# Kernel tuning notes

Measured on AMD Instinct MI355X. Metric: run time of the kernel, lower is better.

Reference implementation:

```python
import jax, jax.numpy as jnp
import numpy as np

T = 2048           # tokens (single prefill sequence)
HIDDEN = 2048
H = 16             # num heads
D_NOPE = 128
D_ROPE = 64
D_V = 128
KV_LORA = 512
EPS = 1e-6
ROPE_THETA = 10000.0


def setup_inputs() -> dict:
    key = jax.random.key(0)
    ks = jax.random.split(key, 7)
    s = 0.02
    return {
        "positions": jnp.arange(T, dtype=jnp.int64) if jax.config.jax_enable_x64 else jnp.arange(T, dtype=jnp.int32),
        "hidden_states": jax.random.normal(ks[0], (T, HIDDEN), dtype=jnp.float32),
        "w_q": jax.random.normal(ks[1], (HIDDEN, H * (D_NOPE + D_ROPE)), dtype=jnp.float32) * s,
        "w_kv_a": jax.random.normal(ks[2], (HIDDEN, KV_LORA + D_ROPE), dtype=jnp.float32) * s,
        "kv_a_ln_w": jax.random.uniform(ks[3], (KV_LORA,), dtype=jnp.float32, minval=0.5, maxval=1.5),
        "w_kv_b": jax.random.normal(ks[4], (KV_LORA, H * (D_NOPE + D_V)), dtype=jnp.float32) * s,
        "w_o": jax.random.normal(ks[5], (H * D_V, HIDDEN), dtype=jnp.float32) * s,
    }


def _rms_norm(x, w):
    var = jnp.mean(jnp.square(x), axis=-1, keepdims=True)
    return x * jax.lax.rsqrt(var + EPS) * w


def _rope_nonneox(x, positions):
    # x: [..., D_ROPE], GPT-J (interleaved) style rotation
    inv_freq = 1.0 / (ROPE_THETA ** (jnp.arange(0, D_ROPE, 2, dtype=jnp.float32) / D_ROPE))
    freqs = positions.astype(jnp.float32)[:, None] * inv_freq  # [T, D_ROPE//2]
    cos, sin = jnp.cos(freqs), jnp.sin(freqs)
    # broadcast over head dim if present
    while cos.ndim < x.ndim:
        cos, sin = cos[:, None], sin[:, None]
    x1, x2 = x[..., 0::2], x[..., 1::2]
    o1 = x1 * cos - x2 * sin
    o2 = x2 * cos + x1 * sin
    return jnp.stack([o1, o2], axis=-1).reshape(x.shape)


def reference(positions, hidden_states, w_q, w_kv_a, kv_a_ln_w, w_kv_b, w_o):
    scaling = (D_NOPE + D_ROPE) ** -0.5
    # q projection (q_lora_rank is None branch)
    q = (hidden_states @ w_q).reshape(T, H, D_NOPE + D_ROPE)
    q_nope, q_pe = q[..., :D_NOPE], q[..., D_NOPE:]
    # compressed KV latent
    latent = hidden_states @ w_kv_a                 # [T, KV_LORA + D_ROPE]
    kv_a = _rms_norm(latent[:, :KV_LORA], kv_a_ln_w)
    k_pe = latent[:, KV_LORA:]                      # [T, D_ROPE], shared across heads
    # decompress to per-head k_nope and v (kv_b_proj)
    kv = (kv_a @ w_kv_b).reshape(T, H, D_NOPE + D_V)
    k_nope, v = kv[..., :D_NOPE], kv[..., D_NOPE:]
    # non-neox RoPE
    q_pe = _rope_nonneox(q_pe, positions)
    k_pe = _rope_nonneox(k_pe, positions)           # [T, D_ROPE]
    # concat rope parts (k_pe broadcast over heads)
    q_full = jnp.concatenate([q_nope, q_pe], axis=-1)                         # [T,H,192]
    k_full = jnp.concatenate([k_nope, jnp.broadcast_to(k_pe[:, None, :], (T, H, D_ROPE))], axis=-1)
    # causal MHA
    scores = jnp.einsum("qhd,khd->hqk", q_full, k_full) * scaling
    causal = positions[:, None] >= positions[None, :]
    scores = jnp.where(causal[None], scores, -jnp.inf)
    attn = jax.nn.softmax(scores, axis=-1)
    out = jnp.einsum("hqk,khd->qhd", attn, v).reshape(T, H * D_V)
    return out @ w_o
```

## Files before the change

kernel.cpp:

```cpp
#include <hip/hip_runtime.h>
#include <hip/hip_bf16.h>
#include <stdint.h>

#define T_SEQ   2048
#define NHEAD   16
#define NPAD1   3712

typedef short bf16x8  __attribute__((ext_vector_type(8)));
typedef float f32x4   __attribute__((ext_vector_type(4)));
typedef float f32x16  __attribute__((ext_vector_type(16)));

__device__ __forceinline__ unsigned short f2bf(float f) {
  union { float f; uint32_t u; } v; v.f = f;
  uint32_t u = v.u;
  uint32_t r = u + 0x7FFF + ((u >> 16) & 1);
  return (unsigned short)(r >> 16);
}

__device__ __forceinline__ void async16(const void* g, void* l) {
  __builtin_amdgcn_global_load_lds(
      (const __attribute__((address_space(1))) void*)g,
      (__attribute__((address_space(3))) void*)l, 16, 0, 0);
}

__device__ __forceinline__ void tr32(const float* __restrict__ in,
    unsigned short* __restrict__ out, int R, int C, int bx, int by,
    float (*tile)[33], int tid) {
  int r0 = bx * 32, c0 = by * 32;
  int tx = tid & 31, ty = tid >> 5;
  for (int i = 0; i < 4; i++)
    tile[ty + i * 8][tx] = in[(size_t)(r0 + ty + i * 8) * C + c0 + tx];
  __syncthreads();
  for (int i = 0; i < 4; i++) {
    int c = ty + i * 8;
    out[(size_t)(c0 + c) * R + r0 + tx] = f2bf(tile[tx][c]);
  }
}

__global__ __launch_bounds__(256) void prep_kernel(
    const float* __restrict__ hs, const float* __restrict__ w_q,
    const float* __restrict__ w_kv_a, const float* __restrict__ w_kv_b,
    const float* __restrict__ w_o, const int* __restrict__ positions,
    unsigned short* __restrict__ hs_bf, unsigned short* __restrict__ wcat_t,
    unsigned short* __restrict__ wkvb_t, unsigned short* __restrict__ wo_t,
    float* __restrict__ rope_tab) {
  __shared__ float tile[32][33];
  int bid = blockIdx.x, tid = threadIdx.x;
  if (bid < 4096) {
    int i = (bid * 256 + tid) * 4;
    float4 v = *(const float4*)(hs + i);
    ushort4 o; o.x = f2bf(v.x); o.y = f2bf(v.y); o.z = f2bf(v.z); o.w = f2bf(v.w);
    *(ushort4*)(hs_bf + i) = o;
  } else if (bid < 4096 + 6144) {
    int l = bid - 4096;
    tr32(w_q, wcat_t, 2048, 3072, l & 63, l >> 6, tile, tid);
  } else if (bid < 4096 + 6144 + 1152) {
    int l = bid - (4096 + 6144);
    tr32(w_kv_a, wcat_t + (size_t)3072 * 2048, 2048, 576, l & 63, l >> 6, tile, tid);
  } else if (bid < 4096 + 6144 + 1152 + 2048) {
    int l = bid - (4096 + 6144 + 1152);
    tr32(w_kv_b, wkvb_t, 512, 4096, l & 15, l >> 4, tile, tid);
  } else if (bid < 4096 + 6144 + 1152 + 2048 + 4096) {
    int l = bid - (4096 + 6144 + 1152 + 2048);
    tr32(w_o, wo_t, 2048, 2048, l & 63, l >> 6, tile, tid);
  } else if (bid < 17600) {
    int l = bid - (4096 + 6144 + 1152 + 2048 + 4096);
    uint4 z = (uint4){0, 0, 0, 0};
    *(uint4*)(wcat_t + (size_t)3648 * 2048 + (size_t)(l * 256 + tid) * 8) = z;
  } else {
    int l = bid - 17600;
    int t = l * 8 + (tid >> 5), p = tid & 31;
    float pos = (float)positions[t];
    float inv_freq = powf(10000.f, -(float)(2 * p) / 64.f);
    float c, s; sincosf(pos * inv_freq, &s, &c);
    rope_tab[(size_t)t * 64 + 2 * p]     = c;
    rope_tab[(size_t)t * 64 + 2 * p + 1] = s;
  }
}

template<int TM, int EPI>
__global__ __launch_bounds__(256) void gemm_bt_kernel(
    const unsigned short* __restrict__ A, const unsigned short* __restrict__ B,
    void* __restrict__ Cv, int M, int N, int K,
    unsigned short* __restrict__ q_full, const float* __restrict__ rope_tab) {
  constexpr int MT = TM / 32;
  __shared__ __align__(16) unsigned short Asm[2][TM * 32];
  __shared__ __align__(16) unsigned short Bsm[2][128 * 32];
  int tid = threadIdx.x, wid = tid >> 6, lane = tid & 63;
  int lrow = lane & 15, lquad = lane >> 4;
  int m0 = blockIdx.x * TM, n0 = blockIdx.y * 128;
  int wm = (wid & 1) * (TM / 2), wn = (wid >> 1) * 64;

  int row_s = tid >> 2, cc_s = tid & 3;
  const unsigned short* Ag0 = A + (size_t)(m0 + row_s) * K + cc_s * 8;
  const unsigned short* Ag1 = A + (size_t)(m0 + row_s + 64) * K + cc_s * 8;
  const unsigned short* Bg0 = B + (size_t)(n0 + row_s) * K + cc_s * 8;
  const unsigned short* Bg1 = B + (size_t)(n0 + row_s + 64) * K + cc_s * 8;

  f32x4 acc[MT][4];
  #pragma unroll
  for (int i = 0; i < MT; i++)
    #pragma unroll
    for (int j = 0; j < 4; j++) acc[i][j] = (f32x4){0.f,0.f,0.f,0.f};

  async16(Ag0, &Asm[0][tid * 8]);
  if (TM == 128) async16(Ag1, &Asm[0][2048 + tid * 8]);
  async16(Bg0, &Bsm[0][tid * 8]);
  async16(Bg1, &Bsm[0][2048 + tid * 8]);

  int cur = 0;
  for (int k0 = 0; k0 < K; k0 += 32) {
    __syncthreads();
    if (k0 + 32 < K) {
      int nxt = cur ^ 1, kk = k0 + 32;
      async16(Ag0 + kk, &Asm[nxt][tid * 8]);
      if (TM == 128) async16(Ag1 + kk, &Asm[nxt][2048 + tid * 8]);
      async16(Bg0 + kk, &Bsm[nxt][tid * 8]);
      async16(Bg1 + kk, &Bsm[nxt][2048 + tid * 8]);
    }
    const unsigned short* As = Asm[cur];
    const unsigned short* Bs = Bsm[cur];
    bf16x8 af[MT], bfr[4];
    #pragma unroll
    for (int mt = 0; mt < MT; mt++)
      af[mt] = *(const bf16x8*)(As + (wm + mt * 16 + lrow) * 32 + lquad * 8);
    #pragma unroll
    for (int nt = 0; nt < 4; nt++)
      bfr[nt] = *(const bf16x8*)(Bs + (wn + nt * 16 + lrow) * 32 + lquad * 8);
    #pragma unroll
    for (int mt = 0; mt < MT; mt++)
      #pragma unroll
      for (int nt = 0; nt < 4; nt++)
        acc[mt][nt] = __builtin_amdgcn_mfma_f32_16x16x32_bf16(af[mt], bfr[nt], acc[mt][nt], 0, 0, 0);
    cur ^= 1;
  }

  if constexpr (EPI == 2) {
    const float scaling = 0.07216878364870323f;
    float* qlat = (float*)Cv;
    #pragma unroll
    for (int nt = 0; nt < 4; nt++) {
      int colb = n0 + wn + nt * 16;
      if (colb >= 3072) {
        int col = colb - 3072 + lrow;
        #pragma unroll
        for (int mt = 0; mt < MT; mt++) {
          int row = m0 + wm + mt * 16 + lquad * 4;
          #pragma unroll
          for (int r = 0; r < 4; r++)
            qlat[(size_t)(row + r) * 640 + col] = acc[mt][nt][r];
        }
      } else {
        int h = colb / 192;
        int hm = colb - h * 192;
        unsigned short* qh = q_full + (size_t)h * T_SEQ * 192;
        if (hm < 128) {
          #pragma unroll
          for (int mt = 0; mt < MT; mt++) {
            int row = m0 + wm + mt * 16 + lquad * 4;
            #pragma unroll
            for (int r = 0; r < 4; r++)
              qh[(size_t)(row + r) * 192 + hm + lrow] = f2bf(acc[mt][nt][r] * scaling);
          }
        } else {
          int p2 = (hm - 128 + lrow) & ~1;
          int odd = lrow & 1;
          #pragma unroll
          for (int mt = 0; mt < MT; mt++) {
            int row = m0 + wm + mt * 16 + lquad * 4;
            #pragma unroll
            for (int r = 0; r < 4; r++) {
              int rg = row + r;
              float c = rope_tab[(size_t)rg * 64 + p2];
              float s = rope_tab[(size_t)rg * 64 + p2 + 1];
              float own = acc[mt][nt][r];
              float oth = __shfl_xor(own, 1, 64);
              float o = odd ? (own * c + oth * s)
                            : (own * c - oth * s);
              qh[(size_t)rg * 192 + hm + lrow] = f2bf(o * scaling);
            }
          }
        }
      }
    }
  } else {
    #pragma unroll
    for (int mt = 0; mt < MT; mt++)
      #pragma unroll
      for (int nt = 0; nt < 4; nt++) {
        int row = m0 + wm + mt * 16 + lquad * 4;
        int col = n0 + wn + nt * 16 + lrow;
        #pragma unroll
        for (int r = 0; r < 4; r++) {
          if (EPI == 1)
            ((unsigned short*)Cv)[(size_t)(row + r) * N + col] = f2bf(acc[mt][nt][r]);
          else
            ((float*)Cv)[(size_t)(row + r) * N + col] = acc[mt][nt][r];
        }
      }
  }
}

__global__ __launch_bounds__(256) void postproc1_kernel(
    const float* __restrict__ q_lat,
    const float* __restrict__ ln_w,
    const float* __restrict__ rope_tab,
    unsigned short* __restrict__ kv_a,
    unsigned short* __restrict__ k_pe)
{
  int t = blockIdx.x, tid = threadIdx.x;
  const float* row = q_lat + (size_t)t * 640;

  float v0 = row[tid], v1 = row[256 + tid];
  float ss = v0 * v0 + v1 * v1;
  for (int m = 1; m < 64; m <<= 1) ss += __shfl_xor(ss, m, 64);
  __shared__ float red[4];
  if ((tid & 63) == 0) red[tid >> 6] = ss;
  __shared__ float kro[64];
  if (tid < 32) {
    float c = rope_tab[(size_t)t * 64 + 2 * tid];
    float s = rope_tab[(size_t)t * 64 + 2 * tid + 1];
    float x1 = row[512 + 2 * tid], x2 = row[512 + 2 * tid + 1];
    kro[2 * tid]     = x1 * c - x2 * s;
    kro[2 * tid + 1] = x2 * c + x1 * s;
  }
  __syncthreads();
  float rstd = rsqrtf((red[0] + red[1] + red[2] + red[3]) * (1.f / 512.f) + 1e-6f);
  kv_a[(size_t)t * 512 + tid]       = f2bf(v0 * rstd * ln_w[tid]);
  kv_a[(size_t)t * 512 + 256 + tid] = f2bf(v1 * rstd * ln_w[256 + tid]);
  if (tid < 64) k_pe[(size_t)t * 64 + tid] = f2bf(kro[tid]);
}

__global__ __launch_bounds__(256) void kvpost_kernel(
    const unsigned short* __restrict__ kv_b,
    unsigned short* __restrict__ v_t) {
  __shared__ unsigned short tile[32][41];
  int l = blockIdx.x, tid = threadIdx.x;
  int h = l >> 8, t0 = (l & 63) * 32, d0 = ((l >> 6) & 3) * 32;
  int tx = tid & 31, ty = tid >> 5;
  for (int i = 0; i < 4; i++)
    tile[ty + i * 8][tx] = kv_b[(size_t)(t0 + ty + i * 8) * 4096 + h * 256 + 128 + d0 + tx];
  __syncthreads();
  for (int i = 0; i < 4; i++)
    v_t[((size_t)h * 128 + d0 + ty + i * 8) * T_SEQ + t0 + tx] = tile[tx][ty + i * 8];
}

#define PP 76
__global__ __launch_bounds__(256, 2) void flash_kernel(
    const unsigned short* __restrict__ q_full,
    const unsigned short* __restrict__ kv_b,
    const unsigned short* __restrict__ k_pe,
    const unsigned short* __restrict__ v_t,
    unsigned short* __restrict__ attn_out)
{
  __shared__ __align__(16) unsigned short Ksm[2][1536 * 8];
  __shared__ __align__(16) unsigned short Vsm[1024 * 8];
  __shared__ __align__(16) unsigned short Psm[64 * PP];
  __shared__ float Lred[2][64];
  int h = blockIdx.x;
  int y = blockIdx.y;
  int qb = (y < 16) ? (31 - y) : (y - 16);
  int tid = threadIdx.x, wid = tid >> 6, lane = tid & 63;
  int l31 = lane & 31, l5 = lane >> 5, x7 = l31 & 7;
  int rq = wid & 1, kq = wid >> 1;

  const unsigned short* vh = v_t + (size_t)h * 128 * T_SEQ;

  const unsigned short* pK[6]; int sK[6];
  #pragma unroll
  for (int j = 0; j < 6; j++) {
    int s = tid + j * 256, row = s / 24, cm = s - row * 24;
    int c = cm ^ (row & 7);
    if (c < 16) { pK[j] = kv_b + (size_t)row * 4096 + h * 256 + c * 8; sK[j] = 64 * 4096; }
    else        { pK[j] = k_pe + (size_t)row * 64 + (c - 16) * 8;      sK[j] = 64 * 64; }
  }
  int gV[4];
  #pragma unroll
  for (int j = 0; j < 4; j++) {
    int s = tid + j * 256, d = s >> 3;
    gV[j] = d * T_SEQ + ((s & 7) ^ (d & 7)) * 8;
  }
  int kxo[12];
  #pragma unroll
  for (int kc = 0; kc < 12; kc++)
    kxo[kc] = (kq * 32 + l31) * 192 + ((kc * 2 + l5) ^ x7) * 8;
  int vxb[2];
  #pragma unroll
  for (int ntv = 0; ntv < 2; ntv++) vxb[ntv] = (kq * 64 + ntv * 32 + l31) * 64;

  bf16x8 qf[12];
  {
    const unsigned short* qrow =
        q_full + ((size_t)h * T_SEQ + qb * 64 + rq * 32 + l31) * 192 + l5 * 8;
    #pragma unroll
    for (int kc = 0; kc < 12; kc++) qf[kc] = *(const bf16x8*)(qrow + kc * 16);
  }
  f32x16 oacc[2];
  for (int i = 0; i < 2; i++) oacc[i] = (f32x16)(0.f);
  float lsum[16];
  #pragma unroll
  for (int r = 0; r < 16; r++) lsum[r] = 0.f;
  int rl[16];
  #pragma unroll
  for (int r = 0; r < 16; r++) rl[r] = (r & 3) + 8 * (r >> 2) + 4 * l5;

  #pragma unroll
  for (int j = 0; j < 6; j++) async16(pK[j], &Ksm[0][(tid + j * 256) * 8]);

  int cur = 0;
  for (int kb = 0; kb <= qb; kb++) {
    __syncthreads();
    {
      const unsigned short* vb = vh + kb * 64;
      #pragma unroll
      for (int j = 0; j < 4; j++) async16(vb + gV[j], &Vsm[(tid + j * 256) * 8]);
    }
    const unsigned short* Ks = Ksm[cur];
    f32x16 sacc = (f32x16)(0.f);
    #pragma unroll
    for (int kc = 0; kc < 12; kc++) {
      bf16x8 kf = *(const bf16x8*)(Ks + kxo[kc]);
      sacc = __builtin_amdgcn_mfma_f32_32x32x16_bf16(qf[kc], kf, sacc, 0, 0, 0);
    }
    if (kb == qb) {
      int col_g = kb * 64 + kq * 32 + l31;
      int row_b = qb * 64 + rq * 32;
      #pragma unroll
      for (int r = 0; r < 16; r++)
        if (col_g > row_b + rl[r]) sacc[r] = -1e30f;
    }
    #pragma unroll
    for (int r = 0; r < 16; r++) {
      float p = __expf(sacc[r]);
      sacc[r] = p;
      lsum[r] += p;
    }
    #pragma unroll
    for (int r = 0; r < 16; r++)
      Psm[(rq * 32 + rl[r]) * PP + kq * 32 + l31] = f2bf(sacc[r]);
    __syncthreads();
    if (kb < qb) {
      #pragma unroll
      for (int j = 0; j < 6; j++)
        async16(pK[j] + (size_t)(kb + 1) * sK[j], &Ksm[cur ^ 1][(tid + j * 256) * 8]);
    }
    #pragma unroll
    for (int kc = 0; kc < 4; kc++) {
      bf16x8 pf = *(const bf16x8*)(Psm + (rq * 32 + l31) * PP + kc * 16 + l5 * 8);
      #pragma unroll
      for (int ntv = 0; ntv < 2; ntv++) {
        bf16x8 vf = *(const bf16x8*)(Vsm + vxb[ntv] + ((kc * 2 + l5) ^ x7) * 8);
        oacc[ntv] = __builtin_amdgcn_mfma_f32_32x32x16_bf16(pf, vf, oacc[ntv], 0, 0, 0);
      }
    }
    cur ^= 1;
  }

  #pragma unroll
  for (int r = 0; r < 16; r++) {
    float s = lsum[r];
    s += __shfl_xor(s, 1, 64);
    s += __shfl_xor(s, 2, 64);
    s += __shfl_xor(s, 4, 64);
    s += __shfl_xor(s, 8, 64);
    s += __shfl_xor(s, 16, 64);
    lsum[r] = s;
  }
  if (l31 == 0)
    #pragma unroll
    for (int r = 0; r < 16; r++) Lred[kq][rq * 32 + rl[r]] = lsum[r];
  __syncthreads();
  #pragma unroll
  for (int r = 0; r < 16; r++) {
    int row_l = rq * 32 + rl[r];
    float inv = 1.f / (Lred[0][row_l] + Lred[1][row_l]);
    int row_g = qb * 64 + row_l;
    #pragma unroll
    for (int ntv = 0; ntv < 2; ntv++)
      attn_out[(size_t)row_g * 2048 + h * 128 + kq * 64 + ntv * 32 + l31] =
          f2bf(oacc[ntv][r] * inv);
  }
}

extern "C" void kernel_launch(void* const* d_in, const int* in_sizes, int n_in,
                              void* d_out, int out_size, void* d_ws, size_t ws_size,
                              hipStream_t stream) {
  const int*   positions = (const int*)d_in[0];
  const float* hs     = (const float*)d_in[1];
  const float* w_q    = (const float*)d_in[2];
  const float* w_kv_a = (const float*)d_in[3];
  const float* ln_w   = (const float*)d_in[4];
  const float* w_kv_b = (const float*)d_in[5];
  const float* w_o    = (const float*)d_in[6];
  float* out = (float*)d_out;

  char* ws = (char*)d_ws;
  size_t off = 0;
  auto alloc = [&](size_t bytes) { void* p = ws + off; off += (bytes + 255) & ~(size_t)255; return p; };
  unsigned short* hs_bf   = (unsigned short*)alloc((size_t)2048 * 2048 * 2);
  unsigned short* wcat_t  = (unsigned short*)alloc((size_t)NPAD1 * 2048 * 2);
  float*          q_lat   = (float*)alloc((size_t)2048 * 640 * 4);
  unsigned short* kv_a_bf = (unsigned short*)alloc((size_t)2048 * 512 * 2);
  unsigned short* wkvb_t  = (unsigned short*)alloc((size_t)4096 * 512 * 2);
  unsigned short* kv_b    = (unsigned short*)alloc((size_t)2048 * 4096 * 2);
  unsigned short* q_full  = (unsigned short*)alloc((size_t)NHEAD * 2048 * 192 * 2);
  unsigned short* k_pe    = (unsigned short*)alloc((size_t)2048 * 64 * 2);
  unsigned short* v_t     = (unsigned short*)alloc((size_t)NHEAD * 128 * 2048 * 2);
  unsigned short* attn_o  = (unsigned short*)alloc((size_t)2048 * 2048 * 2);
  unsigned short* wo_t    = (unsigned short*)alloc((size_t)2048 * 2048 * 2);
  float*          rope_tab= (float*)alloc((size_t)2048 * 64 * 4);

  prep_kernel<<<17856, 256, 0, stream>>>(hs, w_q, w_kv_a, w_kv_b, w_o, positions,
                                         hs_bf, wcat_t, wkvb_t, wo_t, rope_tab);
  gemm_bt_kernel<64, 2><<<dim3(32, 29), 256, 0, stream>>>(
      hs_bf, wcat_t, q_lat, 2048, NPAD1, 2048, q_full, rope_tab);
  postproc1_kernel<<<2048, 256, 0, stream>>>(q_lat, ln_w, rope_tab, kv_a_bf, k_pe);
  gemm_bt_kernel<64, 1><<<dim3(32, 32), 256, 0, stream>>>(
      kv_a_bf, wkvb_t, kv_b, 2048, 4096, 512, nullptr, nullptr);
  kvpost_kernel<<<4096, 256, 0, stream>>>(kv_b, v_t);
  flash_kernel<<<dim3(16, 32), 256, 0, stream>>>(q_full, kv_b, k_pe, v_t, attn_o);
  gemm_bt_kernel<64, 0><<<dim3(32, 16), 256, 0, stream>>>(
      attn_o, wo_t, out, 2048, 2048, 2048, nullptr, nullptr);
}
```

Before: 276.8 us.

## Deepen GEMM K-tile to 64 with XOR-swizzled LDS and larger M tiles

The bf16 GEMM kernel now stages a K-depth of 64 per iteration instead of 32, halving the number of barriers and loop iterations. LDS rows are XOR-swizzled on 16-byte chunks to avoid bank conflicts on the wider rows. The first two GEMMs switch to 128-row M tiles, which halves their grid and increases reuse of each B tile. In exchange, LDS use and register pressure per block go up, and fewer blocks (464 and 512) are spread across the CUs.

```diff
diff --git a/kernel.cpp b/kernel.cpp
--- a/kernel.cpp
+++ b/kernel.cpp
@@ -84,18 +84,21 @@
     void* __restrict__ Cv, int M, int N, int K,
     unsigned short* __restrict__ q_full, const float* __restrict__ rope_tab) {
   constexpr int MT = TM / 32;
-  __shared__ __align__(16) unsigned short Asm[2][TM * 32];
-  __shared__ __align__(16) unsigned short Bsm[2][128 * 32];
+  __shared__ __align__(16) unsigned short Asm[2][TM * 64];
+  __shared__ __align__(16) unsigned short Bsm[2][128 * 64];
   int tid = threadIdx.x, wid = tid >> 6, lane = tid & 63;
   int lrow = lane & 15, lquad = lane >> 4;
   int m0 = blockIdx.x * TM, n0 = blockIdx.y * 128;
   int wm = (wid & 1) * (TM / 2), wn = (wid >> 1) * 64;
 
-  int row_s = tid >> 2, cc_s = tid & 3;
-  const unsigned short* Ag0 = A + (size_t)(m0 + row_s) * K + cc_s * 8;
-  const unsigned short* Ag1 = A + (size_t)(m0 + row_s + 64) * K + cc_s * 8;
-  const unsigned short* Bg0 = B + (size_t)(n0 + row_s) * K + cc_s * 8;
-  const unsigned short* Bg1 = B + (size_t)(n0 + row_s + 64) * K + cc_s * 8;
+  int row_s = tid >> 3;
+  int cc_s = (tid & 7) ^ (row_s & 7);
+  const unsigned short* Ag[MT];
+  const unsigned short* Bg[4];
+  #pragma unroll
+  for (int p = 0; p < MT; p++) Ag[p] = A + (size_t)(m0 + row_s + p * 32) * K + cc_s * 8;
+  #pragma unroll
+  for (int p = 0; p < 4; p++)  Bg[p] = B + (size_t)(n0 + row_s + p * 32) * K + cc_s * 8;
 
   f32x4 acc[MT][4];
   #pragma unroll
@@ -103,35 +106,40 @@
     #pragma unroll
     for (int j = 0; j < 4; j++) acc[i][j] = (f32x4){0.f,0.f,0.f,0.f};
 
-  async16(Ag0, &Asm[0][tid * 8]);
-  if (TM == 128) async16(Ag1, &Asm[0][2048 + tid * 8]);
-  async16(Bg0, &Bsm[0][tid * 8]);
-  async16(Bg1, &Bsm[0][2048 + tid * 8]);
+  #pragma unroll
+  for (int p = 0; p < MT; p++) async16(Ag[p], &Asm[0][(tid + p * 256) * 8]);
+  #pragma unroll
+  for (int p = 0; p < 4; p++)  async16(Bg[p], &Bsm[0][(tid + p * 256) * 8]);
 
   int cur = 0;
-  for (int k0 = 0; k0 < K; k0 += 32) {
+  for (int k0 = 0; k0 < K; k0 += 64) {
     __syncthreads();
-    if (k0 + 32 < K) {
-      int nxt = cur ^ 1, kk = k0 + 32;
-      async16(Ag0 + kk, &Asm[nxt][tid * 8]);
-      if (TM == 128) async16(Ag1 + kk, &Asm[nxt][2048 + tid * 8]);
-      async16(Bg0 + kk, &Bsm[nxt][tid * 8]);
-      async16(Bg1 + kk, &Bsm[nxt][2048 + tid * 8]);
+    if (k0 + 64 < K) {
+      int nxt = cur ^ 1, kk = k0 + 64;
+      #pragma unroll
+      for (int p = 0; p < MT; p++) async16(Ag[p] + kk, &Asm[nxt][(tid + p * 256) * 8]);
+      #pragma unroll
+      for (int p = 0; p < 4; p++)  async16(Bg[p] + kk, &Bsm[nxt][(tid + p * 256) * 8]);
     }
     const unsigned short* As = Asm[cur];
     const unsigned short* Bs = Bsm[cur];
-    bf16x8 af[MT], bfr[4];
-    #pragma unroll
-    for (int mt = 0; mt < MT; mt++)
-      af[mt] = *(const bf16x8*)(As + (wm + mt * 16 + lrow) * 32 + lquad * 8);
-    #pragma unroll
-    for (int nt = 0; nt < 4; nt++)
-      bfr[nt] = *(const bf16x8*)(Bs + (wn + nt * 16 + lrow) * 32 + lquad * 8);
-    #pragma unroll
-    for (int mt = 0; mt < MT; mt++)
+    int xr = (lrow & 7);
+    #pragma unroll
+    for (int kk = 0; kk < 2; kk++) {
+      int cz = ((kk * 4 + lquad) ^ xr) * 8;
+      bf16x8 af[MT], bfr[4];
+      #pragma unroll
+      for (int mt = 0; mt < MT; mt++)
+        af[mt] = *(const bf16x8*)(As + (wm + mt * 16 + lrow) * 64 + cz);
       #pragma unroll
       for (int nt = 0; nt < 4; nt++)
-        acc[mt][nt] = __builtin_amdgcn_mfma_f32_16x16x32_bf16(af[mt], bfr[nt], acc[mt][nt], 0, 0, 0);
+        bfr[nt] = *(const bf16x8*)(Bs + (wn + nt * 16 + lrow) * 64 + cz);
+      #pragma unroll
+      for (int mt = 0; mt < MT; mt++)
+        #pragma unroll
+        for (int nt = 0; nt < 4; nt++)
+          acc[mt][nt] = __builtin_amdgcn_mfma_f32_16x16x32_bf16(af[mt], bfr[nt], acc[mt][nt], 0, 0, 0);
+    }
     cur ^= 1;
   }
 
@@ -412,10 +420,10 @@
 
   prep_kernel<<<17856, 256, 0, stream>>>(hs, w_q, w_kv_a, w_kv_b, w_o, positions,
                                          hs_bf, wcat_t, wkvb_t, wo_t, rope_tab);
-  gemm_bt_kernel<64, 2><<<dim3(32, 29), 256, 0, stream>>>(
+  gemm_bt_kernel<128, 2><<<dim3(16, 29), 256, 0, stream>>>(
       hs_bf, wcat_t, q_lat, 2048, NPAD1, 2048, q_full, rope_tab);
   postproc1_kernel<<<2048, 256, 0, stream>>>(q_lat, ln_w, rope_tab, kv_a_bf, k_pe);
-  gemm_bt_kernel<64, 1><<<dim3(32, 32), 256, 0, stream>>>(
+  gemm_bt_kernel<128, 1><<<dim3(16, 32), 256, 0, stream>>>(
       kv_a_bf, wkvb_t, kv_b, 2048, 4096, 512, nullptr, nullptr);
   kvpost_kernel<<<4096, 256, 0, stream>>>(kv_b, v_t);
   flash_kernel<<<dim3(16, 32), 256, 0, stream>>>(q_full, kv_b, k_pe, v_t, attn_o);
```

Result: faster. 252.7 us (-8.7%).
